# Kernel tuning notes

Measured on AMD Instinct MI355X. Metric: run time of the kernel, lower is better.

The kernel has to match this reference:

```python
import jax, jax.numpy as jnp
import numpy as np

N_NODES = 100000
N_EDGES = 1600000
D = 128


def setup_inputs() -> dict:
    key = jax.random.key(0)
    ks = jax.random.split(key, 6)
    x = jax.random.normal(ks[0], (N_NODES, D), dtype=jnp.float32)
    edge_index = jax.random.randint(ks[1], (2, N_EDGES), 0, N_NODES, dtype=jnp.int32)
    # nn.Linear weights: [out, in], bias [out]
    W1 = jax.random.normal(ks[2], (D, D), dtype=jnp.float32) * (1.0 / np.sqrt(D))
    b1 = jax.random.normal(ks[3], (D,), dtype=jnp.float32) * 0.01
    W2 = jax.random.normal(ks[4], (D, D), dtype=jnp.float32) * (1.0 / np.sqrt(D))
    b2 = jax.random.normal(ks[5], (D,), dtype=jnp.float32) * 0.01
    return {"x": x, "edge_index": edge_index, "W1": W1, "b1": b1, "W2": W2, "b2": b2}


def _gin_conv(x, src, dst, W, b, num_nodes):
    # sum aggregation of source features into destination nodes
    agg = jax.ops.segment_sum(x[src], dst, num_segments=num_nodes)  # [N, d]
    # eps = 0 (PyG GINConv default): (1+eps)*x_i + sum_j x_j, then Linear
    return (x + agg) @ W.T + b


def reference(x, edge_index, W1, b1, W2, b2):
    src, dst = edge_index[0], edge_index[1]
    n = x.shape[0]
    hid = _gin_conv(x, src, dst, W1, b1, n)
    out = _gin_conv(hid, src, dst, W2, b2, n)
    return (out, hid)
```

## Files before the change

kernel.cpp:

```cpp
#include <hip/hip_runtime.h>


#define DFEAT 128
#define BSHIFT 8
#define NB_MAX 512
#define CAP 8192

typedef __attribute__((ext_vector_type(8))) short short8;
typedef __attribute__((ext_vector_type(4))) float f32x4;

__device__ __forceinline__ float bf2f(unsigned short u) {
    union { unsigned int i; float f; } c;
    c.i = ((unsigned int)u) << 16;
    return c.f;
}
__device__ __forceinline__ unsigned short f2b(float f) {
    union { float f; unsigned int i; } c;
    c.f = f;
    unsigned int u = c.i;
    u = (u + 0x7FFFu + ((u >> 16) & 1u)) >> 16;
    return (unsigned short)u;
}


__global__ __launch_bounds__(256) void scatter_cast(const int* __restrict__ src,
                                                    const int* __restrict__ dst,
                                                    int* __restrict__ bcur,
                                                    int* __restrict__ ebuf, int E,
                                                    int nscat,
                                                    const float* __restrict__ x,
                                                    unsigned short* __restrict__ xb,
                                                    int total4) {
    int tid = threadIdx.x;
    if (blockIdx.x >= nscat) {
        int i = (blockIdx.x - nscat) * 256 + tid;
        if (i < total4) {
            float4 v = ((const float4*)x)[i];
            ushort4 o;
            o.x = f2b(v.x); o.y = f2b(v.y); o.z = f2b(v.z); o.w = f2b(v.w);
            ((ushort4*)xb)[i] = o;
        }
        return;
    }
    __shared__ int lh[NB_MAX];
    for (int i = tid; i < NB_MAX; i += 256) lh[i] = 0;
    __syncthreads();
    int e0 = blockIdx.x * 4096;
    int e1 = min(e0 + 4096, E);
    int s[16], d[16];
    #pragma unroll
    for (int j = 0; j < 16; j++) {
        int e = e0 + tid + 256 * j;
        if (e < e1) { s[j] = src[e]; d[j] = dst[e]; atomicAdd(&lh[d[j] >> BSHIFT], 1); }
    }
    __syncthreads();
    for (int i = tid; i < NB_MAX; i += 256) {
        int c = lh[i];
        lh[i] = c ? (i * CAP + atomicAdd(&bcur[i], c)) : 0;
    }
    __syncthreads();
    #pragma unroll
    for (int j = 0; j < 16; j++) {
        int e = e0 + tid + 256 * j;
        if (e < e1) {
            int b = d[j] >> BSHIFT;
            int p = atomicAdd(&lh[b], 1);
            if (p < (b + 1) * CAP) ebuf[p] = (s[j] << 8) | (d[j] & 255);
        }
    }
}


__global__ __launch_bounds__(256) void csr_prep(const int* __restrict__ ebuf,
                                                const int* __restrict__ bcur,
                                                int2* __restrict__ rpse,
                                                int* __restrict__ esrc, int n, int nbk,
                                                const float* __restrict__ W1,
                                                const float* __restrict__ W2,
                                                const float* __restrict__ b1,
                                                unsigned short* __restrict__ Wb1,
                                                unsigned short* __restrict__ Wcb,
                                                float* __restrict__ w2b1) {
    int tid = threadIdx.x;
    if (blockIdx.x >= nbk) {
        __shared__ float red[256];
        int bb = blockIdx.x - nbk;
        int i = bb * 2 + (tid >> 7);
        int j = tid & 127;
        float s = 0.f;
        #pragma unroll 4
        for (int k = 0; k < 128; k++) s += W2[i * 128 + k] * W1[k * 128 + j];
        Wcb[i * 128 + j] = f2b(s);
        Wb1[i * 128 + j] = f2b(W1[i * 128 + j]);
        red[tid] = W2[i * 128 + j] * b1[j];
        __syncthreads();
        if (j == 0) {
            float t = 0.f;
            for (int k = 0; k < 128; k++) t += red[tid + k];
            w2b1[i] = t;
        }
        return;
    }
    __shared__ int hist[256];
    __shared__ int wsum[4];
    __shared__ int woff2[4];
    int b = blockIdx.x;
    int nbase = b << BSHIFT;
    int e0 = b * CAP;
    int e1 = e0 + min(bcur[b], CAP);
    hist[tid] = 0;
    __syncthreads();
    for (int e = e0 + tid; e < e1; e += 256)
        atomicAdd(&hist[ebuf[e] & 255], 1);
    __syncthreads();
    int v = hist[tid];
    int lane = tid & 63, wid = tid >> 6;
    int inc = v;
    #pragma unroll
    for (int off = 1; off < 64; off <<= 1) {
        int u = __shfl_up(inc, off, 64);
        if (lane >= off) inc += u;
    }
    if (lane == 63) wsum[wid] = inc;
    __syncthreads();
    if (tid == 0) {
        int run = 0;
        #pragma unroll
        for (int w = 0; w < 4; w++) { woff2[w] = run; run += wsum[w]; }
    }
    __syncthreads();
    int excl = woff2[wid] + inc - v;
    int node = nbase + tid;
    if (node < n) rpse[node] = make_int2(e0 + excl, e0 + excl + v);
    __syncthreads();
    hist[tid] = excl;
    __syncthreads();
    for (int e = e0 + tid; e < e1; e += 256) {
        int le = ebuf[e];
        int p = atomicAdd(&hist[le & 255], 1);
        esrc[e0 + p] = ((unsigned int)le) >> 8;
    }
}


__device__ __forceinline__ ushort4 agg_node(const char* zb,
                                            const int2* __restrict__ rpse,
                                            const int* __restrict__ esrc,
                                            int node, int n, int hl, int sbase,
                                            unsigned lb) {
    float a0 = 0.f, a1 = 0.f, a2 = 0.f, a3 = 0.f;
    if (node < n) {
        int2 se = rpse[node];
        int e0 = se.x, deg = se.y - se.x;
        ushort4 sv = *(const ushort4*)(zb + ((unsigned)node * 256u + lb));
        a0 = bf2f(sv.x); a1 = bf2f(sv.y); a2 = bf2f(sv.z); a3 = bf2f(sv.w);
        int eidx = (hl < deg) ? esrc[e0 + hl] : 0;
        int m = min(deg, 32);
        int j = 0;
        for (; j + 8 <= m; j += 8) {
            unsigned off[8];
            ushort4 vv[8];
            #pragma unroll
            for (int k = 0; k < 8; k++)
                off[k] = (unsigned)__shfl(eidx, sbase + j + k) * 256u + lb;
            #pragma unroll
            for (int k = 0; k < 8; k++) vv[k] = *(const ushort4*)(zb + off[k]);
            #pragma unroll
            for (int k = 0; k < 8; k++) {
                a0 += bf2f(vv[k].x); a1 += bf2f(vv[k].y);
                a2 += bf2f(vv[k].z); a3 += bf2f(vv[k].w);
            }
        }
        for (; j < m; j++) {
            unsigned off = (unsigned)__shfl(eidx, sbase + j) * 256u + lb;
            ushort4 v = *(const ushort4*)(zb + off);
            a0 += bf2f(v.x); a1 += bf2f(v.y); a2 += bf2f(v.z); a3 += bf2f(v.w);
        }
        for (int e = e0 + 32; e < e0 + deg; e++) {
            unsigned off = (unsigned)esrc[e] * 256u + lb;
            ushort4 v = *(const ushort4*)(zb + off);
            a0 += bf2f(v.x); a1 += bf2f(v.y); a2 += bf2f(v.z); a3 += bf2f(v.w);
        }
    }
    ushort4 o;
    o.x = f2b(a0); o.y = f2b(a1); o.z = f2b(a2); o.w = f2b(a3);
    return o;
}

#define LROWS 136

__global__ __launch_bounds__(256) void fused_agg_gemm1(
        const ushort4* __restrict__ zin4, const int2* __restrict__ rpse,
        const int* __restrict__ esrc, const unsigned short* __restrict__ Wb,
        const float* __restrict__ bias, ushort4* __restrict__ zout4,
        float* __restrict__ out, int n) {
    __shared__ __align__(16) short lt[64 * LROWS];
    int nbase = blockIdx.x * 64;
    int w = threadIdx.x >> 6;
    int hl = threadIdx.x & 31;
    int sbase = threadIdx.x & 32;
    int half = (threadIdx.x >> 5) & 1;
    unsigned lb = (unsigned)hl * 8u;
    const char* zb = (const char*)zin4;
    for (int it = 0; it < 8; ++it) {
        int lrow = w * 16 + it * 2 + half;
        int node = nbase + lrow;
        ushort4 o = agg_node(zb, rpse, esrc, node, n, hl, sbase, lb);
        *(ushort4*)((char*)lt + lrow * (LROWS * 2) + lb) = o;
        if (node < n) zout4[(size_t)node * 32 + hl] = o;
    }
    __syncthreads();
    int lane = threadIdx.x & 63;
    int m = lane & 15, q = lane >> 4;
    const short* ap = lt + (w * 16 + m) * LROWS + q * 8;
    short8 a0 = *(const short8*)(ap);
    short8 a1 = *(const short8*)(ap + 32);
    short8 a2 = *(const short8*)(ap + 64);
    short8 a3 = *(const short8*)(ap + 96);
    f32x4 acc[8];
    #pragma unroll
    for (int c = 0; c < 8; c++) acc[c] = (f32x4){0.f, 0.f, 0.f, 0.f};
    #pragma unroll
    for (int c = 0; c < 8; c++) {
        const short* wp = (const short*)Wb + (c * 16 + m) * 128 + q * 8;
        short8 b0 = *(const short8*)(wp);
        short8 b1v = *(const short8*)(wp + 32);
        short8 b2v = *(const short8*)(wp + 64);
        short8 b3v = *(const short8*)(wp + 96);
        acc[c] = __builtin_amdgcn_mfma_f32_16x16x32_bf16(a0, b0, acc[c], 0, 0, 0);
        acc[c] = __builtin_amdgcn_mfma_f32_16x16x32_bf16(a1, b1v, acc[c], 0, 0, 0);
        acc[c] = __builtin_amdgcn_mfma_f32_16x16x32_bf16(a2, b2v, acc[c], 0, 0, 0);
        acc[c] = __builtin_amdgcn_mfma_f32_16x16x32_bf16(a3, b3v, acc[c], 0, 0, 0);
    }
    int row0 = nbase + w * 16 + q * 4;
    #pragma unroll
    for (int c = 0; c < 8; c++) {
        float bb = bias[c * 16 + m];
        #pragma unroll
        for (int r = 0; r < 4; r++) {
            int node = row0 + r;
            if (node < n) out[(size_t)node * 128 + c * 16 + m] = acc[c][r] + bb;
        }
    }
}

__global__ __launch_bounds__(256) void fused_agg_gemm2(
        const ushort4* __restrict__ zin4, const int2* __restrict__ rpse,
        const int* __restrict__ esrc, const unsigned short* __restrict__ Wb,
        const float* __restrict__ w2b1, const float* __restrict__ bias2,
        float* __restrict__ out, int n) {
    __shared__ __align__(16) short lt[64 * LROWS];
    int nbase = blockIdx.x * 64;
    int w = threadIdx.x >> 6;
    int hl = threadIdx.x & 31;
    int sbase = threadIdx.x & 32;
    int half = (threadIdx.x >> 5) & 1;
    unsigned lb = (unsigned)hl * 8u;
    const char* zb = (const char*)zin4;
    for (int it = 0; it < 8; ++it) {
        int lrow = w * 16 + it * 2 + half;
        int node = nbase + lrow;
        ushort4 o = agg_node(zb, rpse, esrc, node, n, hl, sbase, lb);
        *(ushort4*)((char*)lt + lrow * (LROWS * 2) + lb) = o;
    }
    __syncthreads();
    int lane = threadIdx.x & 63;
    int m = lane & 15, q = lane >> 4;
    const short* ap = lt + (w * 16 + m) * LROWS + q * 8;
    short8 a0 = *(const short8*)(ap);
    short8 a1 = *(const short8*)(ap + 32);
    short8 a2 = *(const short8*)(ap + 64);
    short8 a3 = *(const short8*)(ap + 96);
    f32x4 acc[8];
    #pragma unroll
    for (int c = 0; c < 8; c++) acc[c] = (f32x4){0.f, 0.f, 0.f, 0.f};
    #pragma unroll
    for (int c = 0; c < 8; c++) {
        const short* wp = (const short*)Wb + (c * 16 + m) * 128 + q * 8;
        short8 b0 = *(const short8*)(wp);
        short8 b1v = *(const short8*)(wp + 32);
        short8 b2v = *(const short8*)(wp + 64);
        short8 b3v = *(const short8*)(wp + 96);
        acc[c] = __builtin_amdgcn_mfma_f32_16x16x32_bf16(a0, b0, acc[c], 0, 0, 0);
        acc[c] = __builtin_amdgcn_mfma_f32_16x16x32_bf16(a1, b1v, acc[c], 0, 0, 0);
        acc[c] = __builtin_amdgcn_mfma_f32_16x16x32_bf16(a2, b2v, acc[c], 0, 0, 0);
        acc[c] = __builtin_amdgcn_mfma_f32_16x16x32_bf16(a3, b3v, acc[c], 0, 0, 0);
    }
    int row0 = nbase + w * 16 + q * 4;
    float degf[4];
    #pragma unroll
    for (int r = 0; r < 4; r++) {
        int node = row0 + r;
        if (node < n) {
            int2 se = rpse[node];
            degf[r] = (float)(1 + se.y - se.x);
        } else degf[r] = 0.f;
    }
    #pragma unroll
    for (int c = 0; c < 8; c++) {
        int col = c * 16 + m;
        float wb = w2b1[col];
        float bb = bias2[col];
        #pragma unroll
        for (int r = 0; r < 4; r++) {
            int node = row0 + r;
            if (node < n) out[(size_t)node * 128 + col] = acc[c][r] + degf[r] * wb + bb;
        }
    }
}


extern "C" void kernel_launch(void* const* d_in, const int* in_sizes, int n_in,
                              void* d_out, int out_size, void* d_ws, size_t ws_size,
                              hipStream_t stream) {
    const float* x  = (const float*)d_in[0];
    const int*   ei = (const int*)d_in[1];
    const float* W1 = (const float*)d_in[2];
    const float* b1 = (const float*)d_in[3];
    const float* W2 = (const float*)d_in[4];
    const float* b2 = (const float*)d_in[5];

    const int n = in_sizes[0] / DFEAT;
    const int E = in_sizes[1] / 2;
    const int* src = ei;
    const int* dst = ei + E;
    const int nbuckets = (n + (1 << BSHIFT) - 1) >> BSHIFT;

    float* out = (float*)d_out;
    float* hid = out + (size_t)n * DFEAT;

    unsigned short* xb = (unsigned short*)out;

    char* w = (char*)d_ws;
    const size_t szB = (size_t)n * DFEAT * sizeof(unsigned short);
    unsigned short* z1b = (unsigned short*)w;
    int* ebuf = (int*)(w + szB);
    int* esrc = (int*)(w + 2 * szB);
    int2* rpse = (int2*)(esrc + (size_t)nbuckets * CAP);
    int* bcur = (int*)(rpse + n);
    char* wp = (char*)(bcur + NB_MAX);
    unsigned short* Wb1 = (unsigned short*)wp;
    unsigned short* Wcb = Wb1 + DFEAT * DFEAT;
    float* w2b1 = (float*)(Wcb + DFEAT * DFEAT);

    const int cast_blocks = (n * 32 + 255) / 256;
    hipMemsetAsync(bcur, 0, nbuckets * sizeof(int), stream);
    scatter_cast<<<nbuckets + cast_blocks, 256, 0, stream>>>(
        src, dst, bcur, ebuf, E, nbuckets, x, xb, n * 32);
    csr_prep<<<nbuckets + 64, 256, 0, stream>>>(
        ebuf, bcur, rpse, esrc, n, nbuckets, W1, W2, b1, Wb1, Wcb, w2b1);

    const int gemm_blocks = (n + 63) / 64;
    fused_agg_gemm1<<<gemm_blocks, 256, 0, stream>>>(
        (const ushort4*)xb, rpse, esrc, Wb1, b1, (ushort4*)z1b, hid, n);
    fused_agg_gemm2<<<gemm_blocks, 256, 0, stream>>>(
        (const ushort4*)z1b, rpse, esrc, Wcb, w2b1, b2, out, n);
}
```

Before: 404.0 us.

## Aggregate each node with 16 lanes and 16-byte loads, 16 nodes per block

After: 372.2 us. 7.9% less time.

```diff
diff --git a/kernel.cpp b/kernel.cpp
--- a/kernel.cpp
+++ b/kernel.cpp
@@ -5,6 +5,7 @@
 #define BSHIFT 8
 #define NB_MAX 512
 #define CAP 8192
+#define LROWS 136
 
 typedef __attribute__((ext_vector_type(8))) short short8;
 typedef __attribute__((ext_vector_type(4))) float f32x4;
@@ -30,7 +31,7 @@
                                                     int nscat,
                                                     const float* __restrict__ x,
                                                     unsigned short* __restrict__ xb,
-                                                    int total4) {
+                                                    int total4, int nzero) {
     int tid = threadIdx.x;
     if (blockIdx.x >= nscat) {
         int i = (blockIdx.x - nscat) * 256 + tid;
@@ -40,6 +41,8 @@
             o.x = f2b(v.x); o.y = f2b(v.y); o.z = f2b(v.z); o.w = f2b(v.w);
             ((ushort4*)xb)[i] = o;
         }
+        if (blockIdx.x == nscat && tid < 32)
+            ((ushort4*)xb)[(size_t)nzero * 32 + tid] = make_ushort4(0, 0, 0, 0);
         return;
     }
     __shared__ int lh[NB_MAX];
@@ -143,103 +146,109 @@
 }
 
 
-__device__ __forceinline__ ushort4 agg_node(const char* zb,
-                                            const int2* __restrict__ rpse,
-                                            const int* __restrict__ esrc,
-                                            int node, int n, int hl, int sbase,
-                                            unsigned lb) {
-    float a0 = 0.f, a1 = 0.f, a2 = 0.f, a3 = 0.f;
-    if (node < n) {
-        int2 se = rpse[node];
-        int e0 = se.x, deg = se.y - se.x;
-        ushort4 sv = *(const ushort4*)(zb + ((unsigned)node * 256u + lb));
-        a0 = bf2f(sv.x); a1 = bf2f(sv.y); a2 = bf2f(sv.z); a3 = bf2f(sv.w);
-        int eidx = (hl < deg) ? esrc[e0 + hl] : 0;
-        int m = min(deg, 32);
-        int j = 0;
-        for (; j + 8 <= m; j += 8) {
-            unsigned off[8];
-            ushort4 vv[8];
+__device__ __forceinline__ void agg_node16(const char* __restrict__ zb,
+                                           const int2* __restrict__ rpse,
+                                           const int* __restrict__ esrc,
+                                           int node, int nzero, int gl, int gbase,
+                                           unsigned lb, float a[8]) {
+    int2 se = rpse[node];
+    int e0 = se.x, deg = se.y - se.x;
+    short8 sv = *(const short8*)(zb + (unsigned)node * 256u + lb);
+    #pragma unroll
+    for (int t = 0; t < 8; t++) a[t] = bf2f((unsigned short)sv[t]);
+    int rounds = (deg + 15) >> 4;
+    for (int r = 0; r < rounds; ++r) {
+        int ep = r * 16 + gl;
+        int eidx = (ep < deg) ? esrc[e0 + ep] : nzero;
+        unsigned off[8];
+        short8 vv[8];
+        #pragma unroll
+        for (int k = 0; k < 8; k++)
+            off[k] = (unsigned)__shfl(eidx, gbase + k) * 256u + lb;
+        #pragma unroll
+        for (int k = 0; k < 8; k++) vv[k] = *(const short8*)(zb + off[k]);
+        #pragma unroll
+        for (int k = 0; k < 8; k++) {
             #pragma unroll
-            for (int k = 0; k < 8; k++)
-                off[k] = (unsigned)__shfl(eidx, sbase + j + k) * 256u + lb;
+            for (int t = 0; t < 8; t++) a[t] += bf2f((unsigned short)vv[k][t]);
+        }
+        #pragma unroll
+        for (int k = 0; k < 8; k++)
+            off[k] = (unsigned)__shfl(eidx, gbase + 8 + k) * 256u + lb;
+        #pragma unroll
+        for (int k = 0; k < 8; k++) vv[k] = *(const short8*)(zb + off[k]);
+        #pragma unroll
+        for (int k = 0; k < 8; k++) {
             #pragma unroll
-            for (int k = 0; k < 8; k++) vv[k] = *(const ushort4*)(zb + off[k]);
-            #pragma unroll
-            for (int k = 0; k < 8; k++) {
-                a0 += bf2f(vv[k].x); a1 += bf2f(vv[k].y);
-                a2 += bf2f(vv[k].z); a3 += bf2f(vv[k].w);
-            }
-        }
-        for (; j < m; j++) {
-            unsigned off = (unsigned)__shfl(eidx, sbase + j) * 256u + lb;
-            ushort4 v = *(const ushort4*)(zb + off);
-            a0 += bf2f(v.x); a1 += bf2f(v.y); a2 += bf2f(v.z); a3 += bf2f(v.w);
-        }
-        for (int e = e0 + 32; e < e0 + deg; e++) {
-            unsigned off = (unsigned)esrc[e] * 256u + lb;
-            ushort4 v = *(const ushort4*)(zb + off);
-            a0 += bf2f(v.x); a1 += bf2f(v.y); a2 += bf2f(v.z); a3 += bf2f(v.w);
-        }
-    }
-    ushort4 o;
-    o.x = f2b(a0); o.y = f2b(a1); o.z = f2b(a2); o.w = f2b(a3);
-    return o;
-}
-
-#define LROWS 136
+            for (int t = 0; t < 8; t++) a[t] += bf2f((unsigned short)vv[k][t]);
+        }
+    }
+}
 
 __global__ __launch_bounds__(256) void fused_agg_gemm1(
         const ushort4* __restrict__ zin4, const int2* __restrict__ rpse,
         const int* __restrict__ esrc, const unsigned short* __restrict__ Wb,
-        const float* __restrict__ bias, ushort4* __restrict__ zout4,
+        const float* __restrict__ bias, unsigned short* __restrict__ zout,
         float* __restrict__ out, int n) {
-    __shared__ __align__(16) short lt[64 * LROWS];
-    int nbase = blockIdx.x * 64;
+    __shared__ __align__(16) short lt[16 * LROWS];
+    int nbase = blockIdx.x * 16;
     int w = threadIdx.x >> 6;
-    int hl = threadIdx.x & 31;
-    int sbase = threadIdx.x & 32;
-    int half = (threadIdx.x >> 5) & 1;
-    unsigned lb = (unsigned)hl * 8u;
+    int wl = threadIdx.x & 63;
+    int gl = wl & 15, q = wl >> 4;
+    int gbase = wl & 48;
+    unsigned lb = (unsigned)gl * 16u;
+    int lrow = w * 4 + q;
+    int node = nbase + lrow;
     const char* zb = (const char*)zin4;
-    for (int it = 0; it < 8; ++it) {
-        int lrow = w * 16 + it * 2 + half;
-        int node = nbase + lrow;
-        ushort4 o = agg_node(zb, rpse, esrc, node, n, hl, sbase, lb);
-        *(ushort4*)((char*)lt + lrow * (LROWS * 2) + lb) = o;
-        if (node < n) zout4[(size_t)node * 32 + hl] = o;
-    }
-    __syncthreads();
-    int lane = threadIdx.x & 63;
-    int m = lane & 15, q = lane >> 4;
-    const short* ap = lt + (w * 16 + m) * LROWS + q * 8;
+
+    float a[8];
+    #pragma unroll
+    for (int t = 0; t < 8; t++) a[t] = 0.f;
+    if (node < n) agg_node16(zb, rpse, esrc, node, n, gl, gbase, lb, a);
+    short8 o;
+    #pragma unroll
+    for (int t = 0; t < 8; t++) o[t] = (short)f2b(a[t]);
+    *(short8*)((char*)lt + lrow * (LROWS * 2) + lb) = o;
+    if (node < n) *(short8*)((char*)zout + (unsigned)node * 256u + lb) = o;
+    if (blockIdx.x == 0 && threadIdx.x < 16) {
+        short8 z8;
+        #pragma unroll
+        for (int t = 0; t < 8; t++) z8[t] = 0;
+        *(short8*)((char*)zout + (unsigned)n * 256u + threadIdx.x * 16) = z8;
+    }
+    __syncthreads();
+
+    int m = gl;
+    const short* ap = lt + m * LROWS + q * 8;
     short8 a0 = *(const short8*)(ap);
     short8 a1 = *(const short8*)(ap + 32);
     short8 a2 = *(const short8*)(ap + 64);
     short8 a3 = *(const short8*)(ap + 96);
-    f32x4 acc[8];
-    #pragma unroll
-    for (int c = 0; c < 8; c++) acc[c] = (f32x4){0.f, 0.f, 0.f, 0.f};
-    #pragma unroll
-    for (int c = 0; c < 8; c++) {
+    f32x4 acc[2];
+    #pragma unroll
+    for (int cc = 0; cc < 2; cc++) acc[cc] = (f32x4){0.f, 0.f, 0.f, 0.f};
+    #pragma unroll
+    for (int cc = 0; cc < 2; cc++) {
+        int c = w * 2 + cc;
         const short* wp = (const short*)Wb + (c * 16 + m) * 128 + q * 8;
         short8 b0 = *(const short8*)(wp);
         short8 b1v = *(const short8*)(wp + 32);
         short8 b2v = *(const short8*)(wp + 64);
         short8 b3v = *(const short8*)(wp + 96);
-        acc[c] = __builtin_amdgcn_mfma_f32_16x16x32_bf16(a0, b0, acc[c], 0, 0, 0);
-        acc[c] = __builtin_amdgcn_mfma_f32_16x16x32_bf16(a1, b1v, acc[c], 0, 0, 0);
-        acc[c] = __builtin_amdgcn_mfma_f32_16x16x32_bf16(a2, b2v, acc[c], 0, 0, 0);
-        acc[c] = __builtin_amdgcn_mfma_f32_16x16x32_bf16(a3, b3v, acc[c], 0, 0, 0);
-    }
-    int row0 = nbase + w * 16 + q * 4;
-    #pragma unroll
-    for (int c = 0; c < 8; c++) {
-        float bb = bias[c * 16 + m];
+        acc[cc] = __builtin_amdgcn_mfma_f32_16x16x32_bf16(a0, b0, acc[cc], 0, 0, 0);
+        acc[cc] = __builtin_amdgcn_mfma_f32_16x16x32_bf16(a1, b1v, acc[cc], 0, 0, 0);
+        acc[cc] = __builtin_amdgcn_mfma_f32_16x16x32_bf16(a2, b2v, acc[cc], 0, 0, 0);
+        acc[cc] = __builtin_amdgcn_mfma_f32_16x16x32_bf16(a3, b3v, acc[cc], 0, 0, 0);
+    }
+    int row0 = nbase + q * 4;
+    #pragma unroll
+    for (int cc = 0; cc < 2; cc++) {
+        int col = (w * 2 + cc) * 16 + m;
+        float bb = bias[col];
         #pragma unroll
         for (int r = 0; r < 4; r++) {
-            int node = row0 + r;
-            if (node < n) out[(size_t)node * 128 + c * 16 + m] = acc[c][r] + bb;
+            int nd = row0 + r;
+            if (nd < n) out[(size_t)nd * 128 + col] = acc[cc][r] + bb;
         }
     }
 }
@@ -249,62 +258,68 @@
         const int* __restrict__ esrc, const unsigned short* __restrict__ Wb,
         const float* __restrict__ w2b1, const float* __restrict__ bias2,
         float* __restrict__ out, int n) {
-    __shared__ __align__(16) short lt[64 * LROWS];
-    int nbase = blockIdx.x * 64;
+    __shared__ __align__(16) short lt[16 * LROWS];
+    int nbase = blockIdx.x * 16;
     int w = threadIdx.x >> 6;
-    int hl = threadIdx.x & 31;
-    int sbase = threadIdx.x & 32;
-    int half = (threadIdx.x >> 5) & 1;
-    unsigned lb = (unsigned)hl * 8u;
+    int wl = threadIdx.x & 63;
+    int gl = wl & 15, q = wl >> 4;
+    int gbase = wl & 48;
+    unsigned lb = (unsigned)gl * 16u;
+    int lrow = w * 4 + q;
+    int node = nbase + lrow;
     const char* zb = (const char*)zin4;
-    for (int it = 0; it < 8; ++it) {
-        int lrow = w * 16 + it * 2 + half;
-        int node = nbase + lrow;
-        ushort4 o = agg_node(zb, rpse, esrc, node, n, hl, sbase, lb);
-        *(ushort4*)((char*)lt + lrow * (LROWS * 2) + lb) = o;
-    }
-    __syncthreads();
-    int lane = threadIdx.x & 63;
-    int m = lane & 15, q = lane >> 4;
-    const short* ap = lt + (w * 16 + m) * LROWS + q * 8;
+
+    float a[8];
+    #pragma unroll
+    for (int t = 0; t < 8; t++) a[t] = 0.f;
+    if (node < n) agg_node16(zb, rpse, esrc, node, n, gl, gbase, lb, a);
+    short8 o;
+    #pragma unroll
+    for (int t = 0; t < 8; t++) o[t] = (short)f2b(a[t]);
+    *(short8*)((char*)lt + lrow * (LROWS * 2) + lb) = o;
+    __syncthreads();
+
+    int m = gl;
+    const short* ap = lt + m * LROWS + q * 8;
     short8 a0 = *(const short8*)(ap);
     short8 a1 = *(const short8*)(ap + 32);
     short8 a2 = *(const short8*)(ap + 64);
     short8 a3 = *(const short8*)(ap + 96);
-    f32x4 acc[8];
-    #pragma unroll
-    for (int c = 0; c < 8; c++) acc[c] = (f32x4){0.f, 0.f, 0.f, 0.f};
-    #pragma unroll
-    for (int c = 0; c < 8; c++) {
+    f32x4 acc[2];
+    #pragma unroll
+    for (int cc = 0; cc < 2; cc++) acc[cc] = (f32x4){0.f, 0.f, 0.f, 0.f};
+    #pragma unroll
+    for (int cc = 0; cc < 2; cc++) {
+        int c = w * 2 + cc;
         const short* wp = (const short*)Wb + (c * 16 + m) * 128 + q * 8;
         short8 b0 = *(const short8*)(wp);
         short8 b1v = *(const short8*)(wp + 32);
         short8 b2v = *(const short8*)(wp + 64);
         short8 b3v = *(const short8*)(wp + 96);
-        acc[c] = __builtin_amdgcn_mfma_f32_16x16x32_bf16(a0, b0, acc[c], 0, 0, 0);
-        acc[c] = __builtin_amdgcn_mfma_f32_16x16x32_bf16(a1, b1v, acc[c], 0, 0, 0);
-        acc[c] = __builtin_amdgcn_mfma_f32_16x16x32_bf16(a2, b2v, acc[c], 0, 0, 0);
-        acc[c] = __builtin_amdgcn_mfma_f32_16x16x32_bf16(a3, b3v, acc[c], 0, 0, 0);
-    }
-    int row0 = nbase + w * 16 + q * 4;
+        acc[cc] = __builtin_amdgcn_mfma_f32_16x16x32_bf16(a0, b0, acc[cc], 0, 0, 0);
+        acc[cc] = __builtin_amdgcn_mfma_f32_16x16x32_bf16(a1, b1v, acc[cc], 0, 0, 0);
+        acc[cc] = __builtin_amdgcn_mfma_f32_16x16x32_bf16(a2, b2v, acc[cc], 0, 0, 0);
+        acc[cc] = __builtin_amdgcn_mfma_f32_16x16x32_bf16(a3, b3v, acc[cc], 0, 0, 0);
+    }
+    int row0 = nbase + q * 4;
     float degf[4];
     #pragma unroll
     for (int r = 0; r < 4; r++) {
-        int node = row0 + r;
-        if (node < n) {
-            int2 se = rpse[node];
+        int nd = row0 + r;
+        if (nd < n) {
+            int2 se = rpse[nd];
             degf[r] = (float)(1 + se.y - se.x);
         } else degf[r] = 0.f;
     }
     #pragma unroll
-    for (int c = 0; c < 8; c++) {
-        int col = c * 16 + m;
+    for (int cc = 0; cc < 2; cc++) {
+        int col = (w * 2 + cc) * 16 + m;
         float wb = w2b1[col];
         float bb = bias2[col];
         #pragma unroll
         for (int r = 0; r < 4; r++) {
-            int node = row0 + r;
-            if (node < n) out[(size_t)node * 128 + col] = acc[c][r] + degf[r] * wb + bb;
+            int nd = row0 + r;
+            if (nd < n) out[(size_t)nd * 128 + col] = acc[cc][r] + degf[r] * wb + bb;
         }
     }
 }
@@ -333,9 +348,10 @@
 
     char* w = (char*)d_ws;
     const size_t szB = (size_t)n * DFEAT * sizeof(unsigned short);
+    const size_t szB1 = szB + 4096;
     unsigned short* z1b = (unsigned short*)w;
-    int* ebuf = (int*)(w + szB);
-    int* esrc = (int*)(w + 2 * szB);
+    int* ebuf = (int*)(w + szB1);
+    int* esrc = (int*)(w + szB1 + szB);
     int2* rpse = (int2*)(esrc + (size_t)nbuckets * CAP);
     int* bcur = (int*)(rpse + n);
     char* wp = (char*)(bcur + NB_MAX);
@@ -346,13 +362,13 @@
     const int cast_blocks = (n * 32 + 255) / 256;
     hipMemsetAsync(bcur, 0, nbuckets * sizeof(int), stream);
     scatter_cast<<<nbuckets + cast_blocks, 256, 0, stream>>>(
-        src, dst, bcur, ebuf, E, nbuckets, x, xb, n * 32);
+        src, dst, bcur, ebuf, E, nbuckets, x, xb, n * 32, n);
     csr_prep<<<nbuckets + 64, 256, 0, stream>>>(
         ebuf, bcur, rpse, esrc, n, nbuckets, W1, W2, b1, Wb1, Wcb, w2b1);
 
-    const int gemm_blocks = (n + 63) / 64;
-    fused_agg_gemm1<<<gemm_blocks, 256, 0, stream>>>(
-        (const ushort4*)xb, rpse, esrc, Wb1, b1, (ushort4*)z1b, hid, n);
-    fused_agg_gemm2<<<gemm_blocks, 256, 0, stream>>>(
+    const int fb = (n + 15) / 16;
+    fused_agg_gemm1<<<fb, 256, 0, stream>>>(
+        (const ushort4*)xb, rpse, esrc, Wb1, b1, z1b, hid, n);
+    fused_agg_gemm2<<<fb, 256, 0, stream>>>(
         (const ushort4*)z1b, rpse, esrc, Wcb, w2b1, b2, out, n);
 }
```
